# Performance work log

Hardware: AMD Instinct MI355X
Metric: run time of the kernel (lower is better)

## Reference

```python
import jax, jax.numpy as jnp
import numpy as np

U, I, D, OUT = 8192, 16384, 64, 64

def setup_inputs() -> dict:
    key = jax.random.key(0)
    k1, k2, k3, k4 = jax.random.split(key, 4)
    user_emb = jax.random.normal(k1, (U, D), dtype=jnp.float32)
    item_emb = jax.random.normal(k2, (I, D), dtype=jnp.float32)
    attention_weight = jax.random.normal(k3, (D, OUT), dtype=jnp.float32) * (1.0 / np.sqrt(D))
    adj_matrix = jax.random.randint(k4, (U, I), 0, 2, dtype=jnp.int32)
    return {"user_emb": user_emb, "item_emb": item_emb,
            "attention_weight": attention_weight, "adj_matrix": adj_matrix}

def reference(user_emb, item_emb, attention_weight, adj_matrix):
    # score[u,i] = <user_emb[u], item_emb[i]>  (torch.inner)
    score = jnp.einsum('ud,id->ui', user_emb, item_emb)
    # mask non-edges to 0 (NOT -inf, faithful to torch.where(adj>0, score, 0))
    score = jnp.where(adj_matrix > 0, score, 0.0)
    score = jax.nn.softmax(score, axis=1)
    # flag == True path: aggregate items into users, then project
    output = score @ item_emb          # [U, D]
    output = output @ attention_weight  # [U, OUT]
    return output
```

## Files before the change

kernel.cpp:

```cpp
#include <hip/hip_runtime.h>
#include <hip/hip_bf16.h>
#include <math.h>

#define U_N   8192
#define I_N   16384
#define D_N   64
#define OUT_N 64
#define BM    64
#define BN    64
#define LDS_STRIDE 72

typedef _Float16       half8  __attribute__((ext_vector_type(8)));
typedef short          bf16x8 __attribute__((ext_vector_type(8)));
typedef unsigned short us8v   __attribute__((ext_vector_type(8)));
typedef float          f32x4  __attribute__((ext_vector_type(4)));

static __device__ __forceinline__ unsigned short f2bf(float f) {
    union { __hip_bfloat16 h; unsigned short u; } cv;
    cv.h = __float2bfloat16(f);
    return cv.u;
}

__global__ __launch_bounds__(256, 4)
void atten_main(const float* __restrict__ user_emb,
                const float* __restrict__ item_emb,
                const int*   __restrict__ adj,
                float* __restrict__ wsO,
                float* __restrict__ wsL,
                int items_per_ch, int iters)
{
    __shared__ _Float16       Vn[64 * LDS_STRIDE];
    __shared__ unsigned short Vt[64 * LDS_STRIDE];
    __shared__ unsigned short Pl[4][16 * LDS_STRIDE];

    const int ch   = blockIdx.x;
    const int ub   = blockIdx.y;
    const int t    = threadIdx.x;
    const int w    = t >> 6;
    const int lane = t & 63;
    const int c    = lane & 15;
    const int q    = lane >> 4;

    const int urow0  = ub * BM + w * 16;
    const int ibase0 = ch * items_per_ch;

    half8 ufrag[2];
    {
        const float* up = user_emb + (size_t)(urow0 + c) * D_N + q * 8;
        #pragma unroll
        for (int ks = 0; ks < 2; ++ks) {
            f32x4 a = *(const f32x4*)(up + ks * 32);
            f32x4 b = *(const f32x4*)(up + ks * 32 + 4);
            half8 h;
            #pragma unroll
            for (int j = 0; j < 4; ++j) { h[j] = (_Float16)a[j]; h[4 + j] = (_Float16)b[j]; }
            ufrag[ks] = h;
        }
    }

    f32x4 O[4];
    #pragma unroll
    for (int nt = 0; nt < 4; ++nt) O[nt] = (f32x4){0.f, 0.f, 0.f, 0.f};
    float l_r[4] = {0.f, 0.f, 0.f, 0.f};

    const int*   adjb = adj + (size_t)(urow0 + 4 * q) * I_N + ibase0 + c;
    const float* vnb  = item_emb + (size_t)(ibase0 + (t >> 2)) * D_N + (t & 3) * 16;
    const float* vtb  = item_emb + (size_t)(ibase0 + 16 * w) * D_N + lane;

    int   adj_pf[16];
    f32x4 vn_pf[4];
    float vt_pf[16];

    #pragma unroll
    for (int r = 0; r < 4; ++r)
        #pragma unroll
        for (int nt = 0; nt < 4; ++nt)
            adj_pf[r * 4 + nt] = adjb[(size_t)r * I_N + nt * 16];
    #pragma unroll
    for (int j = 0; j < 4; ++j) vn_pf[j] = *(const f32x4*)(vnb + 4 * j);
    #pragma unroll
    for (int j = 0; j < 16; ++j) vt_pf[j] = vtb[(size_t)j * D_N];

    for (int it = 0; it < iters; ++it) {
        __syncthreads();

        {
            const int r = t >> 2, d0 = (t & 3) * 16;
            half8 h0, h1;
            #pragma unroll
            for (int j = 0; j < 4; ++j) {
                h0[j]     = (_Float16)vn_pf[0][j]; h0[4 + j] = (_Float16)vn_pf[1][j];
                h1[j]     = (_Float16)vn_pf[2][j]; h1[4 + j] = (_Float16)vn_pf[3][j];
            }
            *(half8*)&Vn[r * LDS_STRIDE + d0]     = h0;
            *(half8*)&Vn[r * LDS_STRIDE + d0 + 8] = h1;
        }
        {
            us8v t0, t1;
            #pragma unroll
            for (int j = 0; j < 8; ++j) { t0[j] = f2bf(vt_pf[j]); t1[j] = f2bf(vt_pf[8 + j]); }
            *(us8v*)&Vt[lane * LDS_STRIDE + 16 * w]     = t0;
            *(us8v*)&Vt[lane * LDS_STRIDE + 16 * w + 8] = t1;
        }
        unsigned maskbits = 0;
        #pragma unroll
        for (int k = 0; k < 16; ++k) maskbits |= (adj_pf[k] != 0 ? 1u : 0u) << k;

        if (it + 1 < iters) {
            const size_t ioff = (size_t)(it + 1) * BN;
            #pragma unroll
            for (int r = 0; r < 4; ++r)
                #pragma unroll
                for (int nt = 0; nt < 4; ++nt)
                    adj_pf[r * 4 + nt] = adjb[(size_t)r * I_N + ioff + nt * 16];
            const float* vp = vnb + ioff * D_N;
            #pragma unroll
            for (int j = 0; j < 4; ++j) vn_pf[j] = *(const f32x4*)(vp + 4 * j);
            const float* tp = vtb + ioff * D_N;
            #pragma unroll
            for (int j = 0; j < 16; ++j) vt_pf[j] = tp[(size_t)j * D_N];
        }

        __syncthreads();

        f32x4 S[4];
        #pragma unroll
        for (int nt = 0; nt < 4; ++nt) {
            f32x4 acc = (f32x4){0.f, 0.f, 0.f, 0.f};
            #pragma unroll
            for (int ks = 0; ks < 2; ++ks) {
                half8 bfrag = *(const half8*)&Vn[(16 * nt + c) * LDS_STRIDE + ks * 32 + q * 8];
                acc = __builtin_amdgcn_mfma_f32_16x16x32_f16(ufrag[ks], bfrag, acc, 0, 0, 0);
            }
            S[nt] = acc;
        }

        #pragma unroll
        for (int r = 0; r < 4; ++r)
            #pragma unroll
            for (int nt = 0; nt < 4; ++nt) {
                const float s = ((maskbits >> (r * 4 + nt)) & 1u) ? S[nt][r] : 0.0f;
                const float p = __expf(s);
                S[nt][r] = p;
                l_r[r] += p;
            }

        #pragma unroll
        for (int r = 0; r < 4; ++r)
            #pragma unroll
            for (int nt = 0; nt < 4; ++nt)
                Pl[w][(4 * q + r) * LDS_STRIDE + 16 * nt + c] = f2bf(S[nt][r]);

        #pragma unroll
        for (int ks = 0; ks < 2; ++ks) {
            bf16x8 pfrag = *(const bf16x8*)&Pl[w][c * LDS_STRIDE + ks * 32 + q * 8];
            #pragma unroll
            for (int nt = 0; nt < 4; ++nt) {
                bf16x8 vfrag = *(const bf16x8*)&Vt[(16 * nt + c) * LDS_STRIDE + ks * 32 + q * 8];
                O[nt] = __builtin_amdgcn_mfma_f32_16x16x32_bf16(pfrag, vfrag, O[nt], 0, 0, 0);
            }
        }
    }

    #pragma unroll
    for (int r = 0; r < 4; ++r) {
        float v = l_r[r];
        #pragma unroll
        for (int off = 1; off < 16; off <<= 1) v += __shfl_xor(v, off);
        l_r[r] = v;
    }

    #pragma unroll
    for (int r = 0; r < 4; ++r) {
        const int u = urow0 + 4 * q + r;
        float* dst = wsO + ((size_t)ch * U_N + u) * D_N;
        #pragma unroll
        for (int nt = 0; nt < 4; ++nt)
            dst[16 * nt + c] = O[nt][r];
    }
    if (c == 0) {
        #pragma unroll
        for (int r = 0; r < 4; ++r)
            wsL[(size_t)ch * U_N + urow0 + 4 * q + r] = l_r[r];
    }
}

__global__ __launch_bounds__(256)
void atten_combine(const float* __restrict__ wsO,
                   const float* __restrict__ wsL,
                   const float* __restrict__ attw,
                   float* __restrict__ out,
                   int nch)
{
    __shared__ float inv[64];
    __shared__ float agg[64][68];
    __shared__ float Wl[64][68];

    const int t  = threadIdx.x;
    const int u0 = blockIdx.x * 64;

    {
        const int d = t >> 2, o0 = (t & 3) * 16;
        const float* src = attw + d * OUT_N + o0;
        #pragma unroll
        for (int j = 0; j < 4; ++j)
            *(f32x4*)&Wl[d][o0 + 4 * j] = *(const f32x4*)(src + 4 * j);
    }
    if (t < 64) {
        float L = 0.f;
        for (int cc = 0; cc < nch; ++cc) L += wsL[(size_t)cc * U_N + u0 + t];
        inv[t] = 1.0f / L;
    }
    __syncthreads();

    {
        const int ul = t >> 2, d0 = (t & 3) * 16;
        const int u = u0 + ul;
        f32x4 a4[4];
        #pragma unroll
        for (int j = 0; j < 4; ++j) a4[j] = (f32x4){0.f, 0.f, 0.f, 0.f};
        for (int cc = 0; cc < nch; ++cc) {
            const float* src = wsO + ((size_t)cc * U_N + u) * D_N + d0;
            #pragma unroll
            for (int j = 0; j < 4; ++j) a4[j] += *(const f32x4*)(src + 4 * j);
        }
        const float s = inv[ul];
        #pragma unroll
        for (int j = 0; j < 4; ++j)
            *(f32x4*)&agg[ul][d0 + 4 * j] = a4[j] * s;
    }
    __syncthreads();

    {
        const int ul = t >> 2, o0 = (t & 3) * 16;
        f32x4 acc[4];
        #pragma unroll
        for (int j = 0; j < 4; ++j) acc[j] = (f32x4){0.f, 0.f, 0.f, 0.f};
        for (int d = 0; d < 64; ++d) {
            const float av = agg[ul][d];
            #pragma unroll
            for (int j = 0; j < 4; ++j) {
                f32x4 wv = *(const f32x4*)&Wl[d][o0 + 4 * j];
                acc[j] += wv * av;
            }
        }
        float* dst = out + (size_t)(u0 + ul) * OUT_N + o0;
        #pragma unroll
        for (int j = 0; j < 4; ++j)
            *(f32x4*)(dst + 4 * j) = acc[j];
    }
}

extern "C" void kernel_launch(void* const* d_in, const int* in_sizes, int n_in,
                              void* d_out, int out_size, void* d_ws, size_t ws_size,
                              hipStream_t stream)
{
    const float* user_emb = (const float*)d_in[0];
    const float* item_emb = (const float*)d_in[1];
    const float* attw     = (const float*)d_in[2];
    const int*   adj      = (const int*)d_in[3];
    float* out = (float*)d_out;

    int nch = 8;
    while (nch > 1 && (size_t)nch * U_N * (D_N + 1) * sizeof(float) > ws_size) nch >>= 1;

    float* wsO = (float*)d_ws;
    float* wsL = wsO + (size_t)nch * U_N * D_N;
    const int items_per_ch = I_N / nch;
    const int iters = items_per_ch / BN;

    atten_main<<<dim3(nch, U_N / BM), 256, 0, stream>>>(user_emb, item_emb, adj,
                                                        wsO, wsL, items_per_ch, iters);
    atten_combine<<<dim3(U_N / 64), 256, 0, stream>>>(wsO, wsL, attw, out, nch);
}
```

Measured before the change: 727.9 us.

## Pre-convert item embeddings to fp16/bf16-transposed and read MFMA fragments directly

Adds a prep kernel that converts item embeddings once to an fp16 row-major copy and a bf16 transposed copy in workspace. The main kernel then loads MFMA B-fragments straight from global memory into registers with double-buffered prefetch, dropping the shared-memory staging of items and both block-wide barriers per iteration. The item tile shrinks from 64 to 32 per iteration. The cost is an extra kernel launch, scattered 2-byte transposed stores in the prep kernel, and a removed workspace-size check, so it assumes a large enough workspace.

```diff
diff --git a/kernel.cpp b/kernel.cpp
--- a/kernel.cpp
+++ b/kernel.cpp
@@ -6,13 +6,11 @@
 #define I_N   16384
 #define D_N   64
 #define OUT_N 64
-#define BM    64
-#define BN    64
-#define LDS_STRIDE 72
+#define BN    32
+#define PL_ST 40
 
 typedef _Float16       half8  __attribute__((ext_vector_type(8)));
 typedef short          bf16x8 __attribute__((ext_vector_type(8)));
-typedef unsigned short us8v   __attribute__((ext_vector_type(8)));
 typedef float          f32x4  __attribute__((ext_vector_type(4)));
 
 static __device__ __forceinline__ unsigned short f2bf(float f) {
@@ -21,17 +19,39 @@
     return cv.u;
 }
 
+__global__ __launch_bounds__(256)
+void prep_items(const float* __restrict__ item,
+                _Float16* __restrict__ itemH,
+                unsigned short* __restrict__ itemT)
+{
+    const int i = blockIdx.x * 256 + threadIdx.x;
+    const float* src = item + (size_t)i * D_N;
+    f32x4 v[16];
+    #pragma unroll
+    for (int j = 0; j < 16; ++j) v[j] = *(const f32x4*)(src + 4 * j);
+
+    #pragma unroll
+    for (int j = 0; j < 8; ++j) {
+        half8 h;
+        #pragma unroll
+        for (int k = 0; k < 4; ++k) { h[k] = (_Float16)v[2*j][k]; h[4+k] = (_Float16)v[2*j+1][k]; }
+        *(half8*)&itemH[(size_t)i * D_N + 8 * j] = h;
+    }
+    #pragma unroll
+    for (int d = 0; d < 64; ++d)
+        itemT[(size_t)d * I_N + i] = f2bf(v[d >> 2][d & 3]);
+}
+
 __global__ __launch_bounds__(256, 4)
 void atten_main(const float* __restrict__ user_emb,
-                const float* __restrict__ item_emb,
+                const _Float16* __restrict__ itemH,
+                const unsigned short* __restrict__ itemT,
                 const int*   __restrict__ adj,
                 float* __restrict__ wsO,
                 float* __restrict__ wsL,
                 int items_per_ch, int iters)
 {
-    __shared__ _Float16       Vn[64 * LDS_STRIDE];
-    __shared__ unsigned short Vt[64 * LDS_STRIDE];
-    __shared__ unsigned short Pl[4][16 * LDS_STRIDE];
+    __shared__ unsigned short Pl[4][16 * PL_ST];
 
     const int ch   = blockIdx.x;
     const int ub   = blockIdx.y;
@@ -41,7 +61,7 @@
     const int c    = lane & 15;
     const int q    = lane >> 4;
 
-    const int urow0  = ub * BM + w * 16;
+    const int urow0  = ub * 64 + w * 16;
     const int ibase0 = ch * items_per_ch;
 
     half8 ufrag[2];
@@ -63,110 +83,91 @@
     for (int nt = 0; nt < 4; ++nt) O[nt] = (f32x4){0.f, 0.f, 0.f, 0.f};
     float l_r[4] = {0.f, 0.f, 0.f, 0.f};
 
-    const int*   adjb = adj + (size_t)(urow0 + 4 * q) * I_N + ibase0 + c;
-    const float* vnb  = item_emb + (size_t)(ibase0 + (t >> 2)) * D_N + (t & 3) * 16;
-    const float* vtb  = item_emb + (size_t)(ibase0 + 16 * w) * D_N + lane;
-
-    int   adj_pf[16];
-    f32x4 vn_pf[4];
-    float vt_pf[16];
+    const int*      adjb = adj   + (size_t)(urow0 + 4 * q) * I_N + ibase0 + c;
+    const _Float16* sbb  = itemH + (size_t)(ibase0 + c) * D_N + q * 8;
+    const unsigned short* pvb = itemT + (size_t)c * I_N + ibase0 + q * 8;
+
+    int   adj_pf[2][8];
+    half8 sb_pf[2][4];
 
     #pragma unroll
     for (int r = 0; r < 4; ++r)
         #pragma unroll
-        for (int nt = 0; nt < 4; ++nt)
-            adj_pf[r * 4 + nt] = adjb[(size_t)r * I_N + nt * 16];
-    #pragma unroll
-    for (int j = 0; j < 4; ++j) vn_pf[j] = *(const f32x4*)(vnb + 4 * j);
-    #pragma unroll
-    for (int j = 0; j < 16; ++j) vt_pf[j] = vtb[(size_t)j * D_N];
+        for (int n2 = 0; n2 < 2; ++n2)
+            adj_pf[0][r * 2 + n2] = adjb[(size_t)r * I_N + n2 * 16];
+    #pragma unroll
+    for (int n2 = 0; n2 < 2; ++n2)
+        #pragma unroll
+        for (int ks = 0; ks < 2; ++ks)
+            sb_pf[0][n2 * 2 + ks] = *(const half8*)&sbb[(size_t)(n2 * 16) * D_N + ks * 32];
 
     for (int it = 0; it < iters; ++it) {
-        __syncthreads();
-
-        {
-            const int r = t >> 2, d0 = (t & 3) * 16;
-            half8 h0, h1;
-            #pragma unroll
-            for (int j = 0; j < 4; ++j) {
-                h0[j]     = (_Float16)vn_pf[0][j]; h0[4 + j] = (_Float16)vn_pf[1][j];
-                h1[j]     = (_Float16)vn_pf[2][j]; h1[4 + j] = (_Float16)vn_pf[3][j];
-            }
-            *(half8*)&Vn[r * LDS_STRIDE + d0]     = h0;
-            *(half8*)&Vn[r * LDS_STRIDE + d0 + 8] = h1;
-        }
-        {
-            us8v t0, t1;
-            #pragma unroll
-            for (int j = 0; j < 8; ++j) { t0[j] = f2bf(vt_pf[j]); t1[j] = f2bf(vt_pf[8 + j]); }
-            *(us8v*)&Vt[lane * LDS_STRIDE + 16 * w]     = t0;
-            *(us8v*)&Vt[lane * LDS_STRIDE + 16 * w + 8] = t1;
-        }
-        unsigned maskbits = 0;
-        #pragma unroll
-        for (int k = 0; k < 16; ++k) maskbits |= (adj_pf[k] != 0 ? 1u : 0u) << k;
+        const int    b   = it & 1;
+        const size_t off = (size_t)it * BN;
 
         if (it + 1 < iters) {
-            const size_t ioff = (size_t)(it + 1) * BN;
+            const size_t noff = off + BN;
             #pragma unroll
             for (int r = 0; r < 4; ++r)
                 #pragma unroll
-                for (int nt = 0; nt < 4; ++nt)
-                    adj_pf[r * 4 + nt] = adjb[(size_t)r * I_N + ioff + nt * 16];
-            const float* vp = vnb + ioff * D_N;
-            #pragma unroll
-            for (int j = 0; j < 4; ++j) vn_pf[j] = *(const f32x4*)(vp + 4 * j);
-            const float* tp = vtb + ioff * D_N;
-            #pragma unroll
-            for (int j = 0; j < 16; ++j) vt_pf[j] = tp[(size_t)j * D_N];
-        }
-
-        __syncthreads();
-
-        f32x4 S[4];
-        #pragma unroll
-        for (int nt = 0; nt < 4; ++nt) {
+                for (int n2 = 0; n2 < 2; ++n2)
+                    adj_pf[b ^ 1][r * 2 + n2] = adjb[(size_t)r * I_N + noff + n2 * 16];
+            #pragma unroll
+            for (int n2 = 0; n2 < 2; ++n2)
+                #pragma unroll
+                for (int ks = 0; ks < 2; ++ks)
+                    sb_pf[b ^ 1][n2 * 2 + ks] =
+                        *(const half8*)&sbb[(noff + n2 * 16) * D_N + ks * 32];
+        }
+
+        bf16x8 pv[4];
+        #pragma unroll
+        for (int nt = 0; nt < 4; ++nt)
+            pv[nt] = *(const bf16x8*)&pvb[(size_t)nt * 16 * I_N + off];
+
+        unsigned mask = 0;
+        #pragma unroll
+        for (int k = 0; k < 8; ++k) mask |= (adj_pf[b][k] != 0 ? 1u : 0u) << k;
+
+        f32x4 S[2];
+        #pragma unroll
+        for (int n2 = 0; n2 < 2; ++n2) {
             f32x4 acc = (f32x4){0.f, 0.f, 0.f, 0.f};
             #pragma unroll
-            for (int ks = 0; ks < 2; ++ks) {
-                half8 bfrag = *(const half8*)&Vn[(16 * nt + c) * LDS_STRIDE + ks * 32 + q * 8];
-                acc = __builtin_amdgcn_mfma_f32_16x16x32_f16(ufrag[ks], bfrag, acc, 0, 0, 0);
-            }
-            S[nt] = acc;
+            for (int ks = 0; ks < 2; ++ks)
+                acc = __builtin_amdgcn_mfma_f32_16x16x32_f16(ufrag[ks], sb_pf[b][n2 * 2 + ks],
+                                                             acc, 0, 0, 0);
+            S[n2] = acc;
         }
 
         #pragma unroll
         for (int r = 0; r < 4; ++r)
             #pragma unroll
-            for (int nt = 0; nt < 4; ++nt) {
-                const float s = ((maskbits >> (r * 4 + nt)) & 1u) ? S[nt][r] : 0.0f;
+            for (int n2 = 0; n2 < 2; ++n2) {
+                const float s = ((mask >> (r * 2 + n2)) & 1u) ? S[n2][r] : 0.0f;
                 const float p = __expf(s);
-                S[nt][r] = p;
+                S[n2][r] = p;
                 l_r[r] += p;
             }
 
         #pragma unroll
         for (int r = 0; r < 4; ++r)
             #pragma unroll
-            for (int nt = 0; nt < 4; ++nt)
-                Pl[w][(4 * q + r) * LDS_STRIDE + 16 * nt + c] = f2bf(S[nt][r]);
-
-        #pragma unroll
-        for (int ks = 0; ks < 2; ++ks) {
-            bf16x8 pfrag = *(const bf16x8*)&Pl[w][c * LDS_STRIDE + ks * 32 + q * 8];
-            #pragma unroll
-            for (int nt = 0; nt < 4; ++nt) {
-                bf16x8 vfrag = *(const bf16x8*)&Vt[(16 * nt + c) * LDS_STRIDE + ks * 32 + q * 8];
-                O[nt] = __builtin_amdgcn_mfma_f32_16x16x32_bf16(pfrag, vfrag, O[nt], 0, 0, 0);
-            }
-        }
+            for (int n2 = 0; n2 < 2; ++n2)
+                Pl[w][(4 * q + r) * PL_ST + n2 * 16 + c] = f2bf(S[n2][r]);
+
+        bf16x8 pfrag = *(const bf16x8*)&Pl[w][c * PL_ST + q * 8];
+
+        #pragma unroll
+        for (int nt = 0; nt < 4; ++nt)
+            O[nt] = __builtin_amdgcn_mfma_f32_16x16x32_bf16(pfrag, pv[nt], O[nt], 0, 0, 0);
     }
 
     #pragma unroll
     for (int r = 0; r < 4; ++r) {
         float v = l_r[r];
         #pragma unroll
-        for (int off = 1; off < 16; off <<= 1) v += __shfl_xor(v, off);
+        for (int offx = 1; offx < 16; offx <<= 1) v += __shfl_xor(v, offx);
         l_r[r] = v;
     }
 
@@ -262,14 +263,17 @@
     float* out = (float*)d_out;
 
     int nch = 8;
-    while (nch > 1 && (size_t)nch * U_N * (D_N + 1) * sizeof(float) > ws_size) nch >>= 1;
-
-    float* wsO = (float*)d_ws;
-    float* wsL = wsO + (size_t)nch * U_N * D_N;
+
+    float*          wsO   = (float*)d_ws;
+    float*          wsL   = wsO + (size_t)8 * U_N * D_N;
+    _Float16*       itemH = (_Float16*)(wsL + (size_t)8 * U_N);
+    unsigned short* itemT = (unsigned short*)(itemH + (size_t)I_N * D_N);
+
     const int items_per_ch = I_N / nch;
     const int iters = items_per_ch / BN;
 
-    atten_main<<<dim3(nch, U_N / BM), 256, 0, stream>>>(user_emb, item_emb, adj,
+    prep_items<<<dim3(I_N / 256), 256, 0, stream>>>(item_emb, itemH, itemT);
+    atten_main<<<dim3(nch, U_N / 64), 256, 0, stream>>>(user_emb, itemH, itemT, adj,
                                                         wsO, wsL, items_per_ch, iters);
     atten_combine<<<dim3(U_N / 64), 256, 0, stream>>>(wsO, wsL, attw, out, nch);
 }
```

Result: slower. 1.263 ms (+73.5%).
